# Kernel tuning notes

Measured on AMD Instinct MI355X. Metric: run time of the kernel, lower is better.

Reference implementation:

```python
import jax, jax.numpy as jnp
import numpy as np

DIM = 1024
HEADS = 16
HEAD_DIM = DIM // HEADS
THETA = 10000.0


def _freqs_cis(d, n, theta=THETA):
    # complex rotary frequencies, shape (n, d//2)
    pos = jnp.arange(n, dtype=jnp.float32)
    inv = 1.0 / theta ** (jnp.arange(0, d, 2, dtype=jnp.float32) / d)
    ang = jnp.outer(pos, inv)
    return jax.lax.complex(jnp.cos(ang), jnp.sin(ang))


def _to_complex(x):
    # (..., d) -> (..., d//2) complex via adjacent pairs
    xr = x.astype(jnp.float32).reshape(*x.shape[:-1], -1, 2)
    return jax.lax.complex(xr[..., 0], xr[..., 1])


def _to_real(xc):
    # (..., d//2) complex -> (..., d) interleaved real/imag
    return jnp.stack([jnp.real(xc), jnp.imag(xc)], axis=-1).reshape(*xc.shape[:-1], -1)


def setup_inputs() -> dict:
    key = jax.random.key(0)
    k1, k2, k3 = jax.random.split(key, 3)
    b, seq = 2, 2048
    x = jax.random.normal(k1, (b, DIM, seq), dtype=jnp.float32)
    w_qkv = jax.random.normal(k2, (3 * DIM, DIM), dtype=jnp.float32) * (DIM ** -0.5)
    w_out = jax.random.normal(k3, (DIM, DIM), dtype=jnp.float32) * (DIM ** -0.5)
    return {"x": x, "w_qkv": w_qkv, "w_out": w_out}


def reference(x, w_qkv, w_out):
    b, dim, n = x.shape
    h, hd = HEADS, HEAD_DIM
    scale = hd ** -0.5
    xt = jnp.swapaxes(x, -1, -2)                      # (b, t, dim)
    qkv = jnp.einsum('btd,ed->bte', xt, w_qkv)        # (b, t, 3*dim)
    q, k, v = jnp.split(qkv, 3, axis=-1)
    q = q.reshape(b, n, h, hd)
    k = k.reshape(b, n, h, hd)
    v = v.reshape(b, n, h, hd)
    # rotary embedding on q, k
    fc = _freqs_cis(hd, n)[None, :, None, :]          # (1, t, 1, hd//2)
    q = _to_real(_to_complex(q) * fc).astype(x.dtype)
    k = _to_real(_to_complex(k) * fc).astype(x.dtype)
    # naive full attention
    logits = jnp.einsum('bqhd,bkhd->bhqk', q, k) * scale
    probs = jax.nn.softmax(logits, axis=-1)
    out = jnp.einsum('bhqk,bkhd->bqhd', probs, v)     # (b, t, h, hd)
    out = out.reshape(b, n, dim)
    out = jnp.einsum('btd,ed->bte', out, w_out)       # (b, t, dim)
    return jnp.swapaxes(out, -1, -2)                  # (b, dim, t)
```

## Files before the change

kernel.cpp:

```cpp
#include <hip/hip_runtime.h>
#include <hip/hip_bf16.h>
#include <math.h>

#define B 2
#define N 2048
#define D 1024
#define H 16
#define HD 64

typedef __attribute__((ext_vector_type(8))) short short8;
typedef __attribute__((ext_vector_type(4))) float f32x4;
typedef __attribute__((ext_vector_type(16))) float f32x16;
typedef __attribute__((ext_vector_type(4))) unsigned short ush4;
typedef __attribute__((ext_vector_type(4))) unsigned int uint4v;

__device__ __forceinline__ float bf2f(unsigned short u) {
  unsigned int x = ((unsigned int)u) << 16;
  float f;
  __builtin_memcpy(&f, &x, 4);
  return f;
}
__device__ __forceinline__ unsigned short f2bf(float f) {
  unsigned int x;
  __builtin_memcpy(&x, &f, 4);
  x = x + 0x7fffu + ((x >> 16) & 1u);
  return (unsigned short)(x >> 16);
}
__device__ __forceinline__ unsigned int pk2(float lo, float hi) {
  union { __hip_bfloat162 h; unsigned int u; } cv;
  cv.h = __float22bfloat162_rn(make_float2(lo, hi));
  return cv.u;
}
__device__ __forceinline__ short8 mk_frag(unsigned int w0, unsigned int w1,
                                          unsigned int w2, unsigned int w3) {
  union { uint4v u; short8 s; } cv;
  cv.u = (uint4v){w0, w1, w2, w3};
  return cv.s;
}

__device__ __forceinline__ void gload16(const unsigned short* g, unsigned short* l) {
  __builtin_amdgcn_global_load_lds(
      (const __attribute__((address_space(1))) unsigned int*)(const void*)g,
      (__attribute__((address_space(3))) unsigned int*)(void*)l, 16, 0, 0);
}

__global__ void prep_k(const float* __restrict__ wqkv, unsigned short* __restrict__ wqkv_bf,
                       const float* __restrict__ wout, unsigned short* __restrict__ wout_bf,
                       float2* __restrict__ tab) {
  int blk = blockIdx.x;
  if (blk < 4096) {
    const float* src = (blk < 3072) ? wqkv : wout;
    unsigned short* dst = (blk < 3072) ? wqkv_bf : wout_bf;
    int i = (blk < 3072 ? blk : blk - 3072) * 256 + threadIdx.x;
    float4 v = ((const float4*)src)[i];
    ush4 o;
    o[0] = f2bf(v.x); o[1] = f2bf(v.y); o[2] = f2bf(v.z); o[3] = f2bf(v.w);
    *(ush4*)&dst[i * 4] = o;
  } else {
    int idx = (blk - 4096) * 256 + threadIdx.x;
    int t = idx >> 5, p = idx & 31;
    float inv = powf(10000.f, -(float)p / 32.f);
    float ang = (float)t * inv;
    float s, c;
    sincosf(ang, &s, &c);
    tab[idx] = make_float2(c, s);
  }
}

__global__ __launch_bounds__(256) void transpose_x(const float* __restrict__ x,
                                                   unsigned short* __restrict__ xt) {
  __shared__ float tile[32][33];
  const int tx = threadIdx.x, ty = threadIdx.y;
  const int t0 = blockIdx.x * 32, d0 = blockIdx.y * 32, bb = blockIdx.z;
#pragma unroll
  for (int i = 0; i < 4; ++i) {
    int r = ty * 4 + i;
    tile[r][tx] = x[(size_t)bb * D * N + (size_t)(d0 + r) * N + t0 + tx];
  }
  __syncthreads();
#pragma unroll
  for (int i = 0; i < 4; ++i) {
    int r = ty * 4 + i;
    xt[((size_t)(bb * N) + t0 + r) * D + d0 + tx] = f2bf(tile[tx][r]);
  }
}

template <int MODE>
__global__ __launch_bounds__(256) void gemm_bt(const unsigned short* __restrict__ A,
                                               const unsigned short* __restrict__ Bt,
                                               float* __restrict__ outf,
                                               unsigned short* __restrict__ qkbuf,
                                               unsigned short* __restrict__ vtbuf) {
  __shared__ unsigned short Asm[128 * 64];
  __shared__ unsigned short Bsm[128 * 64];
  const int tid = threadIdx.x;
  const int lane = tid & 63, wid = tid >> 6;
  const int ln = lane & 15, lh = lane >> 4;
  const int wr = wid >> 1, wc = wid & 1;
  const int m0 = blockIdx.x * 128, n0 = blockIdx.y * 128;

  f32x4 acc[4][4];
#pragma unroll
  for (int i = 0; i < 4; ++i)
#pragma unroll
    for (int j = 0; j < 4; ++j) acc[i][j] = (f32x4){0.f, 0.f, 0.f, 0.f};

  for (int k0 = 0; k0 < 1024; k0 += 64) {
#pragma unroll
    for (int jj = 0; jj < 4; ++jj) {
      int slot = tid + jj * 256;
      int row = slot >> 3, u = slot & 7;
      int usw = (u ^ (row & 7)) * 8;
      gload16(&A[(size_t)(m0 + row) * 1024 + k0 + usw], &Asm[slot * 8]);
    }
#pragma unroll
    for (int jj = 0; jj < 4; ++jj) {
      int slot = tid + jj * 256;
      int row = slot >> 3, u = slot & 7;
      int usw = (u ^ (row & 7)) * 8;
      gload16(&Bt[(size_t)(n0 + row) * 1024 + k0 + usw], &Bsm[slot * 8]);
    }
    __syncthreads();
#pragma unroll
    for (int s = 0; s < 2; ++s) {
      short8 af[4], bfr[4];
#pragma unroll
      for (int i = 0; i < 4; ++i) {
        int row = wr * 64 + i * 16 + ln;
        int u = ((s * 4 + lh) ^ (row & 7)) * 8;
        af[i] = *(const short8*)&Asm[row * 64 + u];
      }
#pragma unroll
      for (int j = 0; j < 4; ++j) {
        int row = wc * 64 + j * 16 + ln;
        int u = ((s * 4 + lh) ^ (row & 7)) * 8;
        bfr[j] = *(const short8*)&Bsm[row * 64 + u];
      }
#pragma unroll
      for (int i = 0; i < 4; ++i)
#pragma unroll
        for (int j = 0; j < 4; ++j)
          acc[i][j] = __builtin_amdgcn_mfma_f32_16x16x32_bf16(af[i], bfr[j], acc[i][j], 0, 0, 0);
    }
    __syncthreads();
  }

#pragma unroll
  for (int i = 0; i < 4; ++i) {
    int mrow = m0 + wr * 64 + i * 16 + lh * 4;
    int bb = mrow >> 11, t = mrow & 2047;
#pragma unroll
    for (int j = 0; j < 4; ++j) {
      int e = n0 + wc * 64 + j * 16 + ln;
      if (MODE == 1) {
        float* op = outf + (size_t)bb * D * N + (size_t)e * N + t;
        *(f32x4*)op = acc[i][j];
      } else {
        if (e < 2048) {
#pragma unroll
          for (int jj = 0; jj < 4; ++jj)
            qkbuf[((size_t)(bb * N + t + jj)) * 2048 + e] = f2bf(acc[i][j][jj]);
        } else {
          ush4 v;
#pragma unroll
          for (int jj = 0; jj < 4; ++jj) v[jj] = f2bf(acc[i][j][jj]);
          *(ush4*)&vtbuf[((size_t)bb * 1024 + (e - 2048)) * N + t] = v;
        }
      }
    }
  }
}

__global__ void rope_kernel(unsigned short* __restrict__ qk, const float2* __restrict__ tab) {
  int idx = blockIdx.x * 256 + threadIdx.x;
  int e = (idx & 255) * 8;
  int t = (idx >> 8) & 2047;
  int bb = idx >> 19;
  int p0 = (e & 63) >> 1;
  const float qscl = 0.125f * 1.4426950408889634f;
  float sc = (e < 1024) ? qscl : 1.0f;
  unsigned short* p = qk + ((size_t)(bb * N + t)) * 2048 + e;
  short8 v = *(short8*)p;
#pragma unroll
  for (int q = 0; q < 4; ++q) {
    float2 cs = tab[t * 32 + p0 + q];
    float xe = bf2f((unsigned short)v[2 * q]);
    float xo = bf2f((unsigned short)v[2 * q + 1]);
    v[2 * q] = (short)f2bf((xe * cs.x - xo * cs.y) * sc);
    v[2 * q + 1] = (short)f2bf((xe * cs.y + xo * cs.x) * sc);
  }
  *(short8*)p = v;
}

__global__ __launch_bounds__(256, 2) void attn_kernel(const unsigned short* __restrict__ qk,
                                                      const unsigned short* __restrict__ vt,
                                                      unsigned short* __restrict__ ob) {
  __shared__ unsigned short Ksm[3][64 * 64];
  __shared__ unsigned short Vsm[3][64 * 64];
  const int tid = threadIdx.x;
  const int lane = tid & 63, wid = tid >> 6;
  const int l31 = lane & 31, hi = lane >> 5;
  const int L = blockIdx.x;
  const int hh = L & 31, qb = L >> 5;
  const int bb = hh >> 4, h = hh & 15;
  const unsigned short* Qg = qk + (size_t)bb * N * 2048 + h * 64;
  const unsigned short* Kg = Qg + 1024;
  const unsigned short* Vg = vt + ((size_t)bb * 1024 + h * 64) * N;

  const int q = qb * 128 + wid * 32 + l31;
  short8 qf[4];
#pragma unroll
  for (int c = 0; c < 4; ++c)
    qf[c] = *(const short8*)&Qg[(size_t)q * 2048 + c * 16 + hi * 8];

  f32x16 oL, oH;
#pragma unroll
  for (int r = 0; r < 16; ++r) { oL[r] = 0.f; oH[r] = 0.f; }
  float lrun = 0.f;

  auto STAGE = [&](unsigned short* Kb, unsigned short* Vb, int kb) {
#pragma unroll
    for (int jj = 0; jj < 2; ++jj) {
      int slot = tid + jj * 256;
      int row = slot >> 3, u = slot & 7;
      int usw = (u ^ (row & 7)) * 8;
      gload16(&Kg[(size_t)(kb + row) * 2048 + usw], &Kb[slot * 8]);
    }
#pragma unroll
    for (int jj = 0; jj < 2; ++jj) {
      int slot = tid + jj * 256;
      int row = slot >> 3, u = slot & 7;
      int usw = (u ^ (row & 7)) * 8;
      gload16(&Vg[(size_t)row * N + kb + usw], &Vb[slot * 8]);
    }
  };

  auto COMPUTE = [&](const unsigned short* Kb, const unsigned short* Vb) {
    f32x16 s0, s1;
#pragma unroll
    for (int r = 0; r < 16; ++r) { s0[r] = 0.f; s1[r] = 0.f; }
    __builtin_amdgcn_s_setprio(1);
#pragma unroll
    for (int c = 0; c < 4; ++c) {
      short8 ka = *(const short8*)&Kb[l31 * 64 + (((c * 2 + hi) ^ (l31 & 7)) * 8)];
      s0 = __builtin_amdgcn_mfma_f32_32x32x16_bf16(ka, qf[c], s0, 0, 0, 0);
      int r1 = 32 + l31;
      short8 kb2 = *(const short8*)&Kb[r1 * 64 + (((c * 2 + hi) ^ (r1 & 7)) * 8)];
      s1 = __builtin_amdgcn_mfma_f32_32x32x16_bf16(kb2, qf[c], s1, 0, 0, 0);
    }
    __builtin_amdgcn_s_setprio(0);
    float lsum = 0.f;
#pragma unroll
    for (int r = 0; r < 16; ++r) {
      s0[r] = __builtin_amdgcn_exp2f(s0[r]);
      s1[r] = __builtin_amdgcn_exp2f(s1[r]);
      lsum += s0[r] + s1[r];
    }
    lrun += lsum;
    unsigned int W[16];
#pragma unroll
    for (int i = 0; i < 8; ++i) {
      W[i] = pk2(s0[2 * i], s0[2 * i + 1]);
      W[8 + i] = pk2(s1[2 * i], s1[2 * i + 1]);
    }
    short8 pf[4];
#pragma unroll
    for (int c = 0; c < 4; ++c) {
      unsigned int a0 = W[4 * c + 0], b0 = W[4 * c + 2];
      unsigned int a1 = W[4 * c + 1], b1 = W[4 * c + 3];
      asm volatile("v_permlane32_swap_b32 %0, %1" : "+v"(a0), "+v"(b0));
      asm volatile("v_permlane32_swap_b32 %0, %1" : "+v"(a1), "+v"(b1));
      pf[c] = mk_frag(a0, a1, b0, b1);
    }
    __builtin_amdgcn_s_setprio(1);
#pragma unroll
    for (int c = 0; c < 4; ++c) {
      short8 va = *(const short8*)&Vb[l31 * 64 + (((c * 2 + hi) ^ (l31 & 7)) * 8)];
      oL = __builtin_amdgcn_mfma_f32_32x32x16_bf16(va, pf[c], oL, 0, 0, 0);
      int rH = 32 + l31;
      short8 vb = *(const short8*)&Vb[rH * 64 + (((c * 2 + hi) ^ (rH & 7)) * 8)];
      oH = __builtin_amdgcn_mfma_f32_32x32x16_bf16(vb, pf[c], oH, 0, 0, 0);
    }
    __builtin_amdgcn_s_setprio(0);
  };

  auto ITER = [&](int t, int bc, int bn) {
    __builtin_amdgcn_s_barrier();
    STAGE(Ksm[bn], Vsm[bn], (t + 2) * 64);
    asm volatile("s_waitcnt vmcnt(8)" ::: "memory");
    __builtin_amdgcn_sched_barrier(0);
    __builtin_amdgcn_s_barrier();
    COMPUTE(Ksm[bc], Vsm[bc]);
  };

  STAGE(Ksm[0], Vsm[0], 0);
  STAGE(Ksm[1], Vsm[1], 64);
  for (int tt = 0; tt < 30; tt += 3) {
    ITER(tt + 0, 0, 2);
    ITER(tt + 1, 1, 0);
    ITER(tt + 2, 2, 1);
  }
  __builtin_amdgcn_s_barrier();
  asm volatile("s_waitcnt vmcnt(4)" ::: "memory");
  __builtin_amdgcn_sched_barrier(0);
  __builtin_amdgcn_s_barrier();
  COMPUTE(Ksm[0], Vsm[0]);
  asm volatile("s_waitcnt vmcnt(0)" ::: "memory");
  __builtin_amdgcn_sched_barrier(0);
  __builtin_amdgcn_s_barrier();
  COMPUTE(Ksm[1], Vsm[1]);

  lrun += __shfl_xor(lrun, 32, 64);
  float inv = 1.f / lrun;
  unsigned short* obp = ob + ((size_t)(bb * N + q)) * 1024 + h * 64;
#pragma unroll
  for (int r4 = 0; r4 < 4; ++r4) {
    ush4 vL, vH;
#pragma unroll
    for (int i = 0; i < 4; ++i) {
      vL[i] = f2bf(oL[r4 * 4 + i] * inv);
      vH[i] = f2bf(oH[r4 * 4 + i] * inv);
    }
    *(ush4*)&obp[r4 * 8 + hi * 4] = vL;
    *(ush4*)&obp[32 + r4 * 8 + hi * 4] = vH;
  }
}

extern "C" void kernel_launch(void* const* d_in, const int* in_sizes, int n_in,
                              void* d_out, int out_size, void* d_ws, size_t ws_size,
                              hipStream_t stream) {
  const float* x = (const float*)d_in[0];
  const float* w_qkv = (const float*)d_in[1];
  const float* w_out = (const float*)d_in[2];
  float* out = (float*)d_out;
  char* ws = (char*)d_ws;

  unsigned short* wqkv_bf = (unsigned short*)ws;
  unsigned short* wout_bf = (unsigned short*)(ws + 6291456);
  unsigned short* xt      = (unsigned short*)(ws + 8388608);
  unsigned short* qkbuf   = (unsigned short*)(ws + 16777216);
  unsigned short* vtbuf   = (unsigned short*)(ws + 33554432);
  float2* tab             = (float2*)(ws + 41943040);

  prep_k<<<4352, 256, 0, stream>>>(w_qkv, wqkv_bf, w_out, wout_bf, tab);
  transpose_x<<<dim3(N / 32, D / 32, B), dim3(32, 8), 0, stream>>>(x, xt);

  gemm_bt<0><<<dim3(32, 24), 256, 0, stream>>>(xt, wqkv_bf, nullptr, qkbuf, vtbuf);
  rope_kernel<<<4096, 256, 0, stream>>>(qkbuf, tab);
  attn_kernel<<<512, 256, 0, stream>>>(qkbuf, vtbuf, xt );
  gemm_bt<1><<<dim3(32, 8), 256, 0, stream>>>(xt, wout_bf, out, nullptr, nullptr);
}
```

Before: 127.6 us.

## Load K/V fragments straight from global into registers, drop LDS staging

Removes the triple-buffered shared-memory staging of K and V tiles and the block barriers that went with it. Each wave now reads its MFMA operand fragments directly from global memory into registers, double-buffering K in registers while V is loaded per tile. This removes LDS traffic and barrier synchronisation, but every wave in the block now re-reads the same K/V data from global/L2 (four times the global traffic), and V loads are not prefetched ahead of use, which can expose memory latency.

New measurement: 193.2 us. 51.4% more time.

```diff
diff --git a/kernel.cpp b/kernel.cpp
--- a/kernel.cpp
+++ b/kernel.cpp
@@ -195,8 +195,6 @@
 __global__ __launch_bounds__(256, 2) void attn_kernel(const unsigned short* __restrict__ qk,
                                                       const unsigned short* __restrict__ vt,
                                                       unsigned short* __restrict__ ob) {
-  __shared__ unsigned short Ksm[3][64 * 64];
-  __shared__ unsigned short Vsm[3][64 * 64];
   const int tid = threadIdx.x;
   const int lane = tid & 63, wid = tid >> 6;
   const int l31 = lane & 31, hi = lane >> 5;
@@ -213,40 +211,44 @@
   for (int c = 0; c < 4; ++c)
     qf[c] = *(const short8*)&Qg[(size_t)q * 2048 + c * 16 + hi * 8];
 
+  const unsigned short* KrowA = Kg + (size_t)l31 * 2048 + hi * 8;
+  const unsigned short* KrowB = Kg + (size_t)(32 + l31) * 2048 + hi * 8;
+  const unsigned short* VrowA = Vg + (size_t)l31 * N + hi * 8;
+  const unsigned short* VrowB = Vg + (size_t)(32 + l31) * N + hi * 8;
+
   f32x16 oL, oH;
 #pragma unroll
   for (int r = 0; r < 16; ++r) { oL[r] = 0.f; oH[r] = 0.f; }
   float lrun = 0.f;
 
-  auto STAGE = [&](unsigned short* Kb, unsigned short* Vb, int kb) {
-#pragma unroll
-    for (int jj = 0; jj < 2; ++jj) {
-      int slot = tid + jj * 256;
-      int row = slot >> 3, u = slot & 7;
-      int usw = (u ^ (row & 7)) * 8;
-      gload16(&Kg[(size_t)(kb + row) * 2048 + usw], &Kb[slot * 8]);
-    }
-#pragma unroll
-    for (int jj = 0; jj < 2; ++jj) {
-      int slot = tid + jj * 256;
-      int row = slot >> 3, u = slot & 7;
-      int usw = (u ^ (row & 7)) * 8;
-      gload16(&Vg[(size_t)row * N + kb + usw], &Vb[slot * 8]);
+  auto LDK = [&](short8* kf, int kb) {
+    const unsigned short* pa = KrowA + (size_t)kb * 2048;
+    const unsigned short* pb = KrowB + (size_t)kb * 2048;
+#pragma unroll
+    for (int c = 0; c < 4; ++c) {
+      kf[c] = *(const short8*)(pa + c * 16);
+      kf[4 + c] = *(const short8*)(pb + c * 16);
     }
   };
-
-  auto COMPUTE = [&](const unsigned short* Kb, const unsigned short* Vb) {
+  auto LDV = [&](short8* vf, int kb) {
+    const unsigned short* pa = VrowA + kb;
+    const unsigned short* pb = VrowB + kb;
+#pragma unroll
+    for (int c = 0; c < 4; ++c) {
+      vf[c] = *(const short8*)(pa + c * 16);
+      vf[4 + c] = *(const short8*)(pb + c * 16);
+    }
+  };
+
+  auto TILE = [&](const short8* kf, const short8* vf) {
     f32x16 s0, s1;
 #pragma unroll
     for (int r = 0; r < 16; ++r) { s0[r] = 0.f; s1[r] = 0.f; }
     __builtin_amdgcn_s_setprio(1);
 #pragma unroll
     for (int c = 0; c < 4; ++c) {
-      short8 ka = *(const short8*)&Kb[l31 * 64 + (((c * 2 + hi) ^ (l31 & 7)) * 8)];
-      s0 = __builtin_amdgcn_mfma_f32_32x32x16_bf16(ka, qf[c], s0, 0, 0, 0);
-      int r1 = 32 + l31;
-      short8 kb2 = *(const short8*)&Kb[r1 * 64 + (((c * 2 + hi) ^ (r1 & 7)) * 8)];
-      s1 = __builtin_amdgcn_mfma_f32_32x32x16_bf16(kb2, qf[c], s1, 0, 0, 0);
+      s0 = __builtin_amdgcn_mfma_f32_32x32x16_bf16(kf[c], qf[c], s0, 0, 0, 0);
+      s1 = __builtin_amdgcn_mfma_f32_32x32x16_bf16(kf[4 + c], qf[c], s1, 0, 0, 0);
     }
     __builtin_amdgcn_s_setprio(0);
     float lsum = 0.f;
@@ -275,40 +277,22 @@
     __builtin_amdgcn_s_setprio(1);
 #pragma unroll
     for (int c = 0; c < 4; ++c) {
-      short8 va = *(const short8*)&Vb[l31 * 64 + (((c * 2 + hi) ^ (l31 & 7)) * 8)];
-      oL = __builtin_amdgcn_mfma_f32_32x32x16_bf16(va, pf[c], oL, 0, 0, 0);
-      int rH = 32 + l31;
-      short8 vb = *(const short8*)&Vb[rH * 64 + (((c * 2 + hi) ^ (rH & 7)) * 8)];
-      oH = __builtin_amdgcn_mfma_f32_32x32x16_bf16(vb, pf[c], oH, 0, 0, 0);
+      oL = __builtin_amdgcn_mfma_f32_32x32x16_bf16(vf[c], pf[c], oL, 0, 0, 0);
+      oH = __builtin_amdgcn_mfma_f32_32x32x16_bf16(vf[4 + c], pf[c], oH, 0, 0, 0);
     }
     __builtin_amdgcn_s_setprio(0);
   };
 
-  auto ITER = [&](int t, int bc, int bn) {
-    __builtin_amdgcn_s_barrier();
-    STAGE(Ksm[bn], Vsm[bn], (t + 2) * 64);
-    asm volatile("s_waitcnt vmcnt(8)" ::: "memory");
-    __builtin_amdgcn_sched_barrier(0);
-    __builtin_amdgcn_s_barrier();
-    COMPUTE(Ksm[bc], Vsm[bc]);
-  };
-
-  STAGE(Ksm[0], Vsm[0], 0);
-  STAGE(Ksm[1], Vsm[1], 64);
-  for (int tt = 0; tt < 30; tt += 3) {
-    ITER(tt + 0, 0, 2);
-    ITER(tt + 1, 1, 0);
-    ITER(tt + 2, 2, 1);
-  }
-  __builtin_amdgcn_s_barrier();
-  asm volatile("s_waitcnt vmcnt(4)" ::: "memory");
-  __builtin_amdgcn_sched_barrier(0);
-  __builtin_amdgcn_s_barrier();
-  COMPUTE(Ksm[0], Vsm[0]);
-  asm volatile("s_waitcnt vmcnt(0)" ::: "memory");
-  __builtin_amdgcn_sched_barrier(0);
-  __builtin_amdgcn_s_barrier();
-  COMPUTE(Ksm[1], Vsm[1]);
+  short8 kA[8], kB[8], vf[8];
+  LDK(kA, 0);
+  for (int tt = 0; tt < 32; tt += 2) {
+    LDK(kB, (tt + 1) * 64);
+    LDV(vf, tt * 64);
+    TILE(kA, vf);
+    if (tt + 2 < 32) LDK(kA, (tt + 2) * 64);
+    LDV(vf, (tt + 1) * 64);
+    TILE(kB, vf);
+  }
 
   lrun += __shfl_xor(lrun, 32, 64);
   float inv = 1.f / lrun;
```
